# Kernel tuning notes

Measured on AMD Instinct MI355X. Metric: run time of the kernel, lower is better.

## Reference

```python
import jax, jax.numpy as jnp
import numpy as np

RES = 32
EPS = 0.0


def setup_inputs() -> dict:
    key = jax.random.key(0)
    k1, k2 = jax.random.split(key)
    B, C, N = 32, 64, 8192
    features = jax.random.normal(k1, (B, C, N), dtype=jnp.float32)
    coords = jax.random.normal(k2, (B, 3, N), dtype=jnp.float32)
    return {"features": features, "coords": coords}


def reference(features, coords):
    R = RES
    B, C, N = features.shape
    # center coords per batch (mean over points)
    norm_coords = coords - jnp.mean(coords, axis=2, keepdims=True)  # [B,3,N]
    # normalize=True branch: divide by 2*max point L2 norm
    max_norm = jnp.max(jnp.linalg.norm(norm_coords, axis=1, keepdims=True),
                       axis=2, keepdims=True)  # [B,1,1]
    norm_coords = norm_coords / (max_norm * 2.0 + EPS) + 0.5
    # scale to voxel grid and clip
    norm_coords = jnp.clip(norm_coords * R, 0.0, R - 1)  # [B,3,N]
    vox = jnp.round(norm_coords).astype(jnp.int32)  # [B,3,N]
    # flat voxel index per point, offset per batch -> global segment id
    flat = (vox[:, 0] * R + vox[:, 1]) * R + vox[:, 2]  # [B,N]
    idx = (flat + jnp.arange(B, dtype=jnp.int32)[:, None] * (R ** 3)).reshape(-1)  # [B*N]
    num_seg = B * R ** 3
    cnt = jax.ops.segment_sum(jnp.ones((B * N,), features.dtype), idx,
                              num_segments=num_seg)  # [B*R^3]
    feat_pn = features.transpose(0, 2, 1).reshape(B * N, C)  # [B*N,C]
    sums = jax.ops.segment_sum(feat_pn, idx, num_segments=num_seg)  # [B*R^3,C]
    avg = sums / jnp.maximum(cnt, 1.0)[:, None]
    voxelized = avg.reshape(B, R, R, R, C).transpose(0, 4, 1, 2, 3)  # [B,C,R,R,R]
    return voxelized, norm_coords
```

## Files before the change

### kernel.cpp

```cpp
#include <hip/hip_runtime.h>

constexpr int B = 32, C = 64, N = 8192, R = 32, R3 = R * R * R;
constexpr int HALF = R3 / 2;

constexpr size_t CNT_OFF = 0;
constexpr size_t IDX_OFF = (size_t)B * R3 * 4;
constexpr size_t PRM_OFF = IDX_OFF + (size_t)B * N * 2 + 512;

__global__ __launch_bounds__(1024) void stats_kernel(
    const float* __restrict__ coords, float* __restrict__ params) {
  const int b = blockIdx.x;
  const int t = threadIdx.x;
  const float* cb = coords + (size_t)b * 3 * N;
  __shared__ double sm[1024];
  __shared__ float smf[1024];

  double sx = 0.0, sy = 0.0, sz = 0.0;
  for (int n = t; n < N; n += 1024) {
    sx += (double)cb[n];
    sy += (double)cb[N + n];
    sz += (double)cb[2 * N + n];
  }
  float mean[3];
  double vals[3] = {sx, sy, sz};
  for (int d = 0; d < 3; ++d) {
    sm[t] = vals[d];
    __syncthreads();
    for (int s = 512; s > 0; s >>= 1) {
      if (t < s) sm[t] += sm[t + s];
      __syncthreads();
    }
    mean[d] = (float)(sm[0] / (double)N);
    __syncthreads();
  }

  float mx = 0.0f;
  for (int n = t; n < N; n += 1024) {
    float dx = __fsub_rn(cb[n], mean[0]);
    float dy = __fsub_rn(cb[N + n], mean[1]);
    float dz = __fsub_rn(cb[2 * N + n], mean[2]);
    float n2 = __fadd_rn(__fadd_rn(__fmul_rn(dx, dx), __fmul_rn(dy, dy)),
                         __fmul_rn(dz, dz));
    mx = fmaxf(mx, n2);
  }
  smf[t] = mx;
  __syncthreads();
  for (int s = 512; s > 0; s >>= 1) {
    if (t < s) smf[t] = fmaxf(smf[t], smf[t + s]);
    __syncthreads();
  }
  if (t == 0) {
    float maxn = __fsqrt_rn(smf[0]);
    params[b * 4 + 0] = mean[0];
    params[b * 4 + 1] = mean[1];
    params[b * 4 + 2] = mean[2];
    params[b * 4 + 3] = __fmul_rn(maxn, 2.0f);
  }
}

__global__ __launch_bounds__(256) void voxelize_kernel(
    const float* __restrict__ coords, const float* __restrict__ params,
    float* __restrict__ ncout, unsigned short* __restrict__ idx,
    unsigned int* __restrict__ cnt) {
  const int i = blockIdx.x * 256 + threadIdx.x;
  const int b = i >> 13;
  const int n = i & (N - 1);
  const float* cb = coords + (size_t)b * 3 * N;
  const float m0 = params[b * 4 + 0];
  const float m1 = params[b * 4 + 1];
  const float m2 = params[b * 4 + 2];
  const float dn = params[b * 4 + 3];

  float t0 = __fmul_rn(__fadd_rn(__fdiv_rn(__fsub_rn(cb[n], m0), dn), 0.5f), 32.0f);
  float t1 = __fmul_rn(__fadd_rn(__fdiv_rn(__fsub_rn(cb[N + n], m1), dn), 0.5f), 32.0f);
  float t2 = __fmul_rn(__fadd_rn(__fdiv_rn(__fsub_rn(cb[2 * N + n], m2), dn), 0.5f), 32.0f);
  t0 = fminf(fmaxf(t0, 0.0f), 31.0f);
  t1 = fminf(fmaxf(t1, 0.0f), 31.0f);
  t2 = fminf(fmaxf(t2, 0.0f), 31.0f);

  ncout[(size_t)b * 3 * N + n] = t0;
  ncout[(size_t)b * 3 * N + N + n] = t1;
  ncout[(size_t)b * 3 * N + 2 * N + n] = t2;

  const int vx = (int)rintf(t0);
  const int vy = (int)rintf(t1);
  const int vz = (int)rintf(t2);
  const int flat = (vx * R + vy) * R + vz;
  idx[i] = (unsigned short)flat;
  atomicAdd(&cnt[b * R3 + flat], 1u);
}

__global__ __launch_bounds__(1024) void accum_kernel(
    const float* __restrict__ feats, const unsigned short* __restrict__ idx,
    const unsigned int* __restrict__ cnt, float* __restrict__ voxout) {
  __shared__ float lds[HALF];
  const int blk = blockIdx.x;
  const int h = blk & 1;
  const int c = (blk >> 1) & (C - 1);
  const int b = blk >> 7;
  const int lo = h * HALF;
  const int t = threadIdx.x;

  float4* lp = (float4*)lds;
  float4 z = {0.f, 0.f, 0.f, 0.f};
#pragma unroll
  for (int k = t; k < HALF / 4; k += 1024) lp[k] = z;
  __syncthreads();

  const unsigned short* ib = idx + (size_t)b * N;
  const float* fb = feats + ((size_t)b * C + c) * N;
#pragma unroll
  for (int n = t; n < N; n += 1024) {
    const int flat = (int)ib[n];
    const float f = fb[n];
    const int loc = flat - lo;
    if ((unsigned)loc < (unsigned)HALF) {
      atomicAdd(&lds[loc], f);
    }
  }
  __syncthreads();

  const uint4* cb4 = (const uint4*)(cnt + (size_t)b * R3 + lo);
  float4* ob4 = (float4*)(voxout + ((size_t)b * C + c) * R3 + lo);
#pragma unroll
  for (int v = t; v < HALF / 4; v += 1024) {
    const uint4 k = cb4[v];
    const float4 s = lp[v];
    float4 o;
    o.x = __fdiv_rn(s.x, (float)(k.x ? k.x : 1u));
    o.y = __fdiv_rn(s.y, (float)(k.y ? k.y : 1u));
    o.z = __fdiv_rn(s.z, (float)(k.z ? k.z : 1u));
    o.w = __fdiv_rn(s.w, (float)(k.w ? k.w : 1u));
    ob4[v] = o;
  }
}

extern "C" void kernel_launch(void* const* d_in, const int* in_sizes, int n_in,
                              void* d_out, int out_size, void* d_ws,
                              size_t ws_size, hipStream_t stream) {
  const float* feats  = (const float*)d_in[0];
  const float* coords = (const float*)d_in[1];

  float* voxout = (float*)d_out;
  float* ncout  = voxout + (size_t)B * C * R3;

  char* ws = (char*)d_ws;
  unsigned int* cnt   = (unsigned int*)(ws + CNT_OFF);
  unsigned short* idx = (unsigned short*)(ws + IDX_OFF);
  float* params       = (float*)(ws + PRM_OFF);

  hipMemsetAsync(cnt, 0, (size_t)B * R3 * sizeof(unsigned int), stream);
  stats_kernel<<<B, 1024, 0, stream>>>(coords, params);
  voxelize_kernel<<<(B * N) / 256, 256, 0, stream>>>(coords, params, ncout,
                                                     idx, cnt);
  accum_kernel<<<B * C * 2, 1024, 0, stream>>>(feats, idx, cnt, voxout);
}
```

Measured before the change: 408.3 us.

## Process both voxel halves per block, reusing register-held features and indices

Each accum block now handles one (batch, channel) pair and loops over both halves of the voxel grid, so it no longer needs two blocks per pair. It loads the indices and features into registers once and reuses them for both halves, which halves the global reads of feats and idx. It also adds a launch_bounds occupancy hint of 8. In exchange there is half as many blocks, the two halves run one after the other within a block, and there are extra barriers.

```diff
diff --git a/kernel.cpp b/kernel.cpp
--- a/kernel.cpp
+++ b/kernel.cpp
@@ -2,6 +2,8 @@
 
 constexpr int B = 32, C = 64, N = 8192, R = 32, R3 = R * R * R;
 constexpr int HALF = R3 / 2;
+constexpr int T = 1024;
+constexpr int PPT = N / T;
 
 constexpr size_t CNT_OFF = 0;
 constexpr size_t IDX_OFF = (size_t)B * R3 * 4;
@@ -90,48 +92,57 @@
   atomicAdd(&cnt[b * R3 + flat], 1u);
 }
 
-__global__ __launch_bounds__(1024) void accum_kernel(
+__global__ __launch_bounds__(1024, 8) void accum_kernel(
     const float* __restrict__ feats, const unsigned short* __restrict__ idx,
     const unsigned int* __restrict__ cnt, float* __restrict__ voxout) {
   __shared__ float lds[HALF];
   const int blk = blockIdx.x;
-  const int h = blk & 1;
-  const int c = (blk >> 1) & (C - 1);
-  const int b = blk >> 7;
-  const int lo = h * HALF;
+  const int c = blk & (C - 1);
+  const int b = blk >> 6;
   const int t = threadIdx.x;
-
-  float4* lp = (float4*)lds;
-  float4 z = {0.f, 0.f, 0.f, 0.f};
-#pragma unroll
-  for (int k = t; k < HALF / 4; k += 1024) lp[k] = z;
-  __syncthreads();
 
   const unsigned short* ib = idx + (size_t)b * N;
   const float* fb = feats + ((size_t)b * C + c) * N;
+  int iv[PPT];
+  float fv[PPT];
 #pragma unroll
-  for (int n = t; n < N; n += 1024) {
-    const int flat = (int)ib[n];
-    const float f = fb[n];
-    const int loc = flat - lo;
-    if ((unsigned)loc < (unsigned)HALF) {
-      atomicAdd(&lds[loc], f);
+  for (int k = 0; k < PPT; ++k) {
+    const int n = t + k * T;
+    iv[k] = (int)ib[n];
+    fv[k] = fb[n];
+  }
+
+  float4* lp = (float4*)lds;
+  const float4 z = {0.f, 0.f, 0.f, 0.f};
+
+  for (int h = 0; h < 2; ++h) {
+    const int lo = h * HALF;
+
+#pragma unroll
+    for (int k = t; k < HALF / 4; k += T) lp[k] = z;
+    __syncthreads();
+
+#pragma unroll
+    for (int k = 0; k < PPT; ++k) {
+      const int loc = iv[k] - lo;
+      if ((unsigned)loc < (unsigned)HALF) atomicAdd(&lds[loc], fv[k]);
     }
-  }
-  __syncthreads();
+    __syncthreads();
 
-  const uint4* cb4 = (const uint4*)(cnt + (size_t)b * R3 + lo);
-  float4* ob4 = (float4*)(voxout + ((size_t)b * C + c) * R3 + lo);
+    const uint4* cb4 = (const uint4*)(cnt + (size_t)b * R3 + lo);
+    float4* ob4 = (float4*)(voxout + ((size_t)b * C + c) * R3 + lo);
 #pragma unroll
-  for (int v = t; v < HALF / 4; v += 1024) {
-    const uint4 k = cb4[v];
-    const float4 s = lp[v];
-    float4 o;
-    o.x = __fdiv_rn(s.x, (float)(k.x ? k.x : 1u));
-    o.y = __fdiv_rn(s.y, (float)(k.y ? k.y : 1u));
-    o.z = __fdiv_rn(s.z, (float)(k.z ? k.z : 1u));
-    o.w = __fdiv_rn(s.w, (float)(k.w ? k.w : 1u));
-    ob4[v] = o;
+    for (int v = t; v < HALF / 4; v += T) {
+      const uint4 k4 = cb4[v];
+      const float4 s = lp[v];
+      float4 o;
+      o.x = __fdiv_rn(s.x, (float)(k4.x ? k4.x : 1u));
+      o.y = __fdiv_rn(s.y, (float)(k4.y ? k4.y : 1u));
+      o.z = __fdiv_rn(s.z, (float)(k4.z ? k4.z : 1u));
+      o.w = __fdiv_rn(s.w, (float)(k4.w ? k4.w : 1u));
+      ob4[v] = o;
+    }
+    __syncthreads();
   }
 }
 
@@ -153,5 +164,5 @@
   stats_kernel<<<B, 1024, 0, stream>>>(coords, params);
   voxelize_kernel<<<(B * N) / 256, 256, 0, stream>>>(coords, params, ncout,
                                                      idx, cnt);
-  accum_kernel<<<B * C * 2, 1024, 0, stream>>>(feats, idx, cnt, voxout);
+  accum_kernel<<<B * C, 1024, 0, stream>>>(feats, idx, cnt, voxout);
 }
```

Result: faster. 395.7 us (-3.1%).
